# Performance work log

Hardware: AMD Instinct MI355X
Metric: run time of the kernel (lower is better)

Reference implementation:

```python
import jax, jax.numpy as jnp
import numpy as np

NEG_SLOPE = 0.2


def gat_layer(x, src, dst, W, a_src, a_dst, b, n_nodes):
    # x: [N, F_in]; W: [F_in, H*C]; a_src/a_dst: [H, C]; b: [H*C]
    H, C = a_src.shape
    h = (x @ W).reshape(n_nodes, H, C)                    # [N, H, C]
    al_s = jnp.sum(h * a_src, axis=-1)                    # [N, H]
    al_d = jnp.sum(h * a_dst, axis=-1)                    # [N, H]
    e = jax.nn.leaky_relu(al_s[src] + al_d[dst], NEG_SLOPE)  # [E, H]
    # segment softmax over incoming edges of each dst node
    m = jax.ops.segment_max(e, dst, num_segments=n_nodes)   # [N, H]
    e = jnp.exp(e - m[dst])
    s = jax.ops.segment_sum(e, dst, num_segments=n_nodes)   # [N, H]
    alpha = e / (s[dst] + 1e-16)                             # [E, H]
    msg = h[src] * alpha[:, :, None]                         # [E, H, C]
    out = jax.ops.segment_sum(msg, dst, num_segments=n_nodes)
    return out.reshape(n_nodes, H * C) + b


def setup_inputs() -> dict:
    key = jax.random.key(0)
    ks = jax.random.split(key, 16)
    N, E = 50000, 800000
    F_in, Hd, heads, n_cls = 256, 256, 8, 64
    C = Hd // heads
    x = jax.random.normal(ks[0], (N, F_in), dtype=jnp.float32)
    edge_index = jax.random.randint(ks[1], (2, E), 0, N, dtype=jnp.int64)

    def lin(k, fin, fout):
        return jax.random.normal(k, (fin, fout), dtype=jnp.float32) / np.sqrt(fin).astype(np.float32)

    inp = {"x": x, "edge_index": edge_index}
    # layer 1: 256 -> 8 heads x 32
    inp["W1"] = lin(ks[2], F_in, Hd)
    inp["as1"] = jax.random.normal(ks[3], (heads, C), dtype=jnp.float32) * 0.1
    inp["ad1"] = jax.random.normal(ks[4], (heads, C), dtype=jnp.float32) * 0.1
    inp["b1"] = jnp.zeros((Hd,), dtype=jnp.float32)
    # layer 2: 256 -> 8 heads x 32
    inp["W2"] = lin(ks[5], Hd, Hd)
    inp["as2"] = jax.random.normal(ks[6], (heads, C), dtype=jnp.float32) * 0.1
    inp["ad2"] = jax.random.normal(ks[7], (heads, C), dtype=jnp.float32) * 0.1
    inp["b2"] = jnp.zeros((Hd,), dtype=jnp.float32)
    # layer 3: 256 -> 1 head x 64 (num_classes)
    inp["W3"] = lin(ks[8], Hd, n_cls)
    inp["as3"] = jax.random.normal(ks[9], (1, n_cls), dtype=jnp.float32) * 0.1
    inp["ad3"] = jax.random.normal(ks[10], (1, n_cls), dtype=jnp.float32) * 0.1
    inp["b3"] = jnp.zeros((n_cls,), dtype=jnp.float32)
    return inp


def reference(x, edge_index, W1, as1, ad1, b1, W2, as2, ad2, b2, W3, as3, ad3, b3):
    N = x.shape[0]
    # PyG GATConv default add_self_loops=True
    loop = jnp.arange(N, dtype=edge_index.dtype)
    src = jnp.concatenate([edge_index[0], loop])
    dst = jnp.concatenate([edge_index[1], loop])
    h = gat_layer(x, src, dst, W1, as1, ad1, b1, N)
    h = jax.nn.relu(h)  # dropout is identity at inference
    h = gat_layer(h, src, dst, W2, as2, ad2, b2, N)
    h = jax.nn.relu(h)
    out = gat_layer(h, src, dst, W3, as3, ad3, b3, N)
    return out
```

## Files before the change

kernel.cpp:

```cpp
#include <hip/hip_runtime.h>
#include <math.h>

#define NSLOPE 0.2f

typedef __attribute__((ext_vector_type(8))) short bf16x8;
typedef __attribute__((ext_vector_type(8))) unsigned short ushort8;
typedef __attribute__((ext_vector_type(4))) float f32x4;

static __device__ __forceinline__ float leaky(float e) {
    return e > 0.f ? e : NSLOPE * e;
}

static __device__ __forceinline__ float bfu(unsigned short u) {
    return __uint_as_float(((unsigned)u) << 16);
}

static __device__ __forceinline__ unsigned short f2bf_rne(float f) {
    unsigned b = __float_as_uint(f);
    unsigned r = b + 0x7fffu + ((b >> 16) & 1u);
    return (unsigned short)(r >> 16);
}

static __device__ __forceinline__ void split1(float f, unsigned short& hi,
                                              unsigned short& lo) {
    unsigned b = __float_as_uint(f);
    unsigned hb = b & 0xffff0000u;
    hi = (unsigned short)(hb >> 16);
    lo = (unsigned short)(__float_as_uint(f - __uint_as_float(hb)) >> 16);
}


__global__ void k_scan_local(const int* __restrict__ cnt, int* __restrict__ ptr,
                             int* __restrict__ bsum, int N) {
    __shared__ int sd[256];
    int t = threadIdx.x;
    int i0 = blockIdx.x * 1024 + t * 4;
    int v0 = (i0 + 0 < N) ? cnt[i0 + 0] + 1 : 0;
    int v1 = (i0 + 1 < N) ? cnt[i0 + 1] + 1 : 0;
    int v2 = (i0 + 2 < N) ? cnt[i0 + 2] + 1 : 0;
    int v3 = (i0 + 3 < N) ? cnt[i0 + 3] + 1 : 0;
    int ts = v0 + v1 + v2 + v3;
    sd[t] = ts;
    __syncthreads();
    for (int o = 1; o < 256; o <<= 1) {
        int add = (t >= o) ? sd[t - o] : 0;
        __syncthreads();
        sd[t] += add;
        __syncthreads();
    }
    int run = sd[t] - ts;
    if (i0 + 0 < N) ptr[i0 + 0] = run; run += v0;
    if (i0 + 1 < N) ptr[i0 + 1] = run; run += v1;
    if (i0 + 2 < N) ptr[i0 + 2] = run; run += v2;
    if (i0 + 3 < N) ptr[i0 + 3] = run;
    if (t == 255) bsum[blockIdx.x] = sd[255];
}

__global__ void k_scan_add2(int* __restrict__ ptr, int* __restrict__ fptr,
                            const int* __restrict__ bsum, int N, int Et) {
    __shared__ int base;
    const int chunk = blockIdx.x >> 2;
    if (threadIdx.x == 0) {
        int s = 0;
        for (int b = 0; b < chunk; ++b) s += bsum[b];
        base = s;
    }
    __syncthreads();
    int i = blockIdx.x * 256 + threadIdx.x;
    if (i < N) {
        int v = ptr[i] + base;
        ptr[i] = v;
        fptr[i] = v;
    } else if (i == N) {
        ptr[N] = Et;
    }
}

__global__ void k_fillcsr(const int* __restrict__ ei, int* __restrict__ fptr,
                          int* __restrict__ srcs, int E, int Et) {
    int i = blockIdx.x * blockDim.x + threadIdx.x;
    if (i >= Et) return;
    int s, d;
    if (i < E) { s = ei[i]; d = ei[E + i]; }
    else       { s = d = i - E; }
    int pos = atomicAdd(&fptr[d], 1);
    srcs[pos] = s;
}

__global__ __launch_bounds__(256) void k_prep(
    const int* __restrict__ ei_dst, int* __restrict__ cnt, int E, int N,
    const float* __restrict__ x, unsigned short* __restrict__ xhi,
    unsigned short* __restrict__ xlo, int n8,
    const float* __restrict__ W1, unsigned short* __restrict__ w1h, unsigned short* __restrict__ w1l,
    const float* __restrict__ W2, unsigned short* __restrict__ w2h, unsigned short* __restrict__ w2l,
    const float* __restrict__ W3, unsigned short* __restrict__ w3h, unsigned short* __restrict__ w3l,
    int ncnt, int nsplit) {
    __shared__ float tile[32][33];
    const int b = blockIdx.x;
    const int tid = threadIdx.x;
    if (b < ncnt) {
        int i = b * 256 + tid;
        if (i < E) atomicAdd(&cnt[ei_dst[i]], 1);
    } else if (b < ncnt + nsplit) {
        int i = (b - ncnt) * 256 + tid;
        if (i < n8) {
            const float4 v0 = *reinterpret_cast<const float4*>(&x[(size_t)i * 8]);
            const float4 v1 = *reinterpret_cast<const float4*>(&x[(size_t)i * 8 + 4]);
            const float f[8] = {v0.x, v0.y, v0.z, v0.w, v1.x, v1.y, v1.z, v1.w};
            ushort8 h, l;
#pragma unroll
            for (int j = 0; j < 8; ++j) {
                unsigned short hj, lj;
                split1(f[j], hj, lj);
                h[j] = hj; l[j] = lj;
            }
            *reinterpret_cast<ushort8*>(&xhi[(size_t)i * 8]) = h;
            *reinterpret_cast<ushort8*>(&xlo[(size_t)i * 8]) = l;
        }
    } else {
        int tb = b - ncnt - nsplit;
        const float* B; unsigned short *H, *L;
        int M, bx, by;
        if (tb < 64)       { B = W1; H = w1h; L = w1l; M = 256; bx = (tb & 7) * 32; by = (tb >> 3) * 32; }
        else if (tb < 128) { tb -= 64;  B = W2; H = w2h; L = w2l; M = 256; bx = (tb & 7) * 32; by = (tb >> 3) * 32; }
        else               { tb -= 128; B = W3; H = w3h; L = w3l; M = 64;  bx = (tb & 1) * 32; by = (tb >> 1) * 32; }
        constexpr int K = 256;
        const int tx = tid & 31, ty = tid >> 5;
        for (int r = ty; r < 32; r += 8) tile[r][tx] = B[(size_t)(by + r) * M + bx + tx];
        __syncthreads();
        for (int r = ty; r < 32; r += 8) {
            unsigned short h, l;
            split1(tile[tx][r], h, l);
            H[(size_t)(bx + r) * K + by + tx] = h;
            L[(size_t)(bx + r) * K + by + tx] = l;
        }
    }
}

__global__ __launch_bounds__(256) void k_gemm2(const unsigned short* __restrict__ Ahi,
                                               const unsigned short* __restrict__ Alo,
                                               const unsigned short* __restrict__ Whi,
                                               const unsigned short* __restrict__ Wlo,
                                               const float* __restrict__ asrc,
                                               const float* __restrict__ adst,
                                               unsigned short* __restrict__ hb,
                                               float* __restrict__ als,
                                               float* __restrict__ ald,
                                               int N) {
    constexpr int K = 256;
    constexpr int M = 256;
    __shared__ unsigned short Ah[64][36], Al[64][36];
    __shared__ unsigned short Bh[256][36], Bl[256][36];
    const int tid = threadIdx.x;
    const int lane = tid & 63;
    const int wid = tid >> 6;
    const int row0 = blockIdx.x * 64;

    const int sr = tid >> 2;
    const int sk = (tid & 3) << 3;
    const int ga = row0 + sr;
    const size_t gaK = (size_t)ga * K;

    const int wc0 = wid * 64;
    const int fr = lane & 15;
    const int ko = (lane >> 4) * 8;

    f32x4 acc[4][4];
#pragma unroll
    for (int i = 0; i < 4; ++i)
#pragma unroll
        for (int j = 0; j < 4; ++j) acc[i][j] = (f32x4){0.f, 0.f, 0.f, 0.f};

    for (int k0 = 0; k0 < K; k0 += 32) {
        ushort8 ah = {0,0,0,0,0,0,0,0}, al = {0,0,0,0,0,0,0,0};
        if (ga < N) {
            ah = *reinterpret_cast<const ushort8*>(&Ahi[gaK + k0 + sk]);
            al = *reinterpret_cast<const ushort8*>(&Alo[gaK + k0 + sk]);
        }
        *reinterpret_cast<ushort8*>(&Ah[sr][sk]) = ah;
        *reinterpret_cast<ushort8*>(&Al[sr][sk]) = al;
#pragma unroll
        for (int p = 0; p < 4; ++p) {
            const int m = sr + 64 * p;
            const size_t gm = (size_t)m * K + k0 + sk;
            *reinterpret_cast<ushort8*>(&Bh[m][sk]) =
                *reinterpret_cast<const ushort8*>(&Whi[gm]);
            *reinterpret_cast<ushort8*>(&Bl[m][sk]) =
                *reinterpret_cast<const ushort8*>(&Wlo[gm]);
        }
        __syncthreads();

        bf16x8 ahi[4], alo4[4];
#pragma unroll
        for (int i = 0; i < 4; ++i) {
            ahi[i]  = *reinterpret_cast<const bf16x8*>(&Ah[i * 16 + fr][ko]);
            alo4[i] = *reinterpret_cast<const bf16x8*>(&Al[i * 16 + fr][ko]);
        }
#pragma unroll
        for (int j = 0; j < 4; ++j) {
            const bf16x8 bh = *reinterpret_cast<const bf16x8*>(&Bh[wc0 + j * 16 + fr][ko]);
            const bf16x8 bl = *reinterpret_cast<const bf16x8*>(&Bl[wc0 + j * 16 + fr][ko]);
#pragma unroll
            for (int i = 0; i < 4; ++i) {
                acc[i][j] = __builtin_amdgcn_mfma_f32_16x16x32_bf16(ahi[i], bh, acc[i][j], 0, 0, 0);
                acc[i][j] = __builtin_amdgcn_mfma_f32_16x16x32_bf16(ahi[i], bl, acc[i][j], 0, 0, 0);
                acc[i][j] = __builtin_amdgcn_mfma_f32_16x16x32_bf16(alo4[i], bh, acc[i][j], 0, 0, 0);
            }
        }
        __syncthreads();
    }

    const int orow = (lane >> 4) * 4;
    const int ocol = lane & 15;

#pragma unroll
    for (int i = 0; i < 4; ++i) {
#pragma unroll
        for (int r = 0; r < 4; ++r) {
            const int row = row0 + i * 16 + orow + r;
            if (row < N) {
#pragma unroll
                for (int j = 0; j < 4; ++j) {
                    const int col = wc0 + j * 16 + ocol;
                    hb[(size_t)row * M + col] = f2bf_rne(acc[i][j][r]);
                }
            }
        }
    }

    const float as0 = asrc[wc0 + ocol],      as1 = asrc[wc0 + 16 + ocol];
    const float as2 = asrc[wc0 + 32 + ocol], as3 = asrc[wc0 + 48 + ocol];
    const float ad0 = adst[wc0 + ocol],      ad1 = adst[wc0 + 16 + ocol];
    const float ad2 = adst[wc0 + 32 + ocol], ad3 = adst[wc0 + 48 + ocol];
    const int headA = wc0 >> 5, headB = headA + 1;

#pragma unroll
    for (int i = 0; i < 4; ++i) {
#pragma unroll
        for (int r = 0; r < 4; ++r) {
            float psA = acc[i][0][r] * as0 + acc[i][1][r] * as1;
            float pdA = acc[i][0][r] * ad0 + acc[i][1][r] * ad1;
            float psB = acc[i][2][r] * as2 + acc[i][3][r] * as3;
            float pdB = acc[i][2][r] * ad2 + acc[i][3][r] * ad3;
#pragma unroll
            for (int o = 1; o < 16; o <<= 1) {
                psA += __shfl_xor(psA, o);
                pdA += __shfl_xor(pdA, o);
                psB += __shfl_xor(psB, o);
                pdB += __shfl_xor(pdB, o);
            }
            const int row = row0 + i * 16 + orow + r;
            if (ocol == 0 && row < N) {
                als[(size_t)row * 8 + headA] = psA;
                ald[(size_t)row * 8 + headA] = pdA;
                als[(size_t)row * 8 + headB] = psB;
                ald[(size_t)row * 8 + headB] = pdB;
            }
        }
    }
}


template <int HN, int CN>
__global__ __launch_bounds__(256) void k_gemm_s(const unsigned short* __restrict__ Ahi,
                                                const unsigned short* __restrict__ Alo,
                                                const unsigned short* __restrict__ Whi,
                                                const unsigned short* __restrict__ Wlo,
                                                const float* __restrict__ asrc,
                                                const float* __restrict__ adst,
                                                unsigned short* __restrict__ hb,
                                                float* __restrict__ als,
                                                float* __restrict__ ald,
                                                int N) {
    constexpr int K = 256;
    constexpr int M = HN * CN;
    __shared__ unsigned short Ah[64][40], Al[64][40], Bh[64][40], Bl[64][40];
    const int tid = threadIdx.x;
    const int lane = tid & 63;
    const int wid = tid >> 6;
    const int row0 = blockIdx.x * 64;
    const int col0 = blockIdx.y * 64;

    const int sr = tid >> 2;
    const int sk = (tid & 3) << 3;
    const int ga = row0 + sr;
    const size_t gaK = (size_t)ga * K;
    const size_t gcK = (size_t)(col0 + sr) * K;

    const int wr = (wid >> 1) * 32;
    const int wc = (wid & 1) * 32;
    const int fr = lane & 15;
    const int ko = (lane >> 4) * 8;

    f32x4 acc[2][2];
#pragma unroll
    for (int i = 0; i < 2; ++i)
#pragma unroll
        for (int j = 0; j < 2; ++j) acc[i][j] = (f32x4){0.f, 0.f, 0.f, 0.f};

    for (int k0 = 0; k0 < K; k0 += 32) {
        ushort8 ah = {0,0,0,0,0,0,0,0}, al = {0,0,0,0,0,0,0,0};
        if (ga < N) {
            ah = *reinterpret_cast<const ushort8*>(&Ahi[gaK + k0 + sk]);
            al = *reinterpret_cast<const ushort8*>(&Alo[gaK + k0 + sk]);
        }
        const ushort8 bh = *reinterpret_cast<const ushort8*>(&Whi[gcK + k0 + sk]);
        const ushort8 bl = *reinterpret_cast<const ushort8*>(&Wlo[gcK + k0 + sk]);
        *reinterpret_cast<ushort8*>(&Ah[sr][sk]) = ah;
        *reinterpret_cast<ushort8*>(&Al[sr][sk]) = al;
        *reinterpret_cast<ushort8*>(&Bh[sr][sk]) = bh;
        *reinterpret_cast<ushort8*>(&Bl[sr][sk]) = bl;
        __syncthreads();

        bf16x8 ahi[2], alo[2], bhi[2], blo[2];
#pragma unroll
        for (int i = 0; i < 2; ++i) {
            ahi[i] = *reinterpret_cast<const bf16x8*>(&Ah[wr + i * 16 + fr][ko]);
            alo[i] = *reinterpret_cast<const bf16x8*>(&Al[wr + i * 16 + fr][ko]);
        }
#pragma unroll
        for (int j = 0; j < 2; ++j) {
            bhi[j] = *reinterpret_cast<const bf16x8*>(&Bh[wc + j * 16 + fr][ko]);
            blo[j] = *reinterpret_cast<const bf16x8*>(&Bl[wc + j * 16 + fr][ko]);
        }
#pragma unroll
        for (int i = 0; i < 2; ++i)
#pragma unroll
            for (int j = 0; j < 2; ++j) {
                acc[i][j] = __builtin_amdgcn_mfma_f32_16x16x32_bf16(ahi[i], bhi[j], acc[i][j], 0, 0, 0);
                acc[i][j] = __builtin_amdgcn_mfma_f32_16x16x32_bf16(ahi[i], blo[j], acc[i][j], 0, 0, 0);
                acc[i][j] = __builtin_amdgcn_mfma_f32_16x16x32_bf16(alo[i], bhi[j], acc[i][j], 0, 0, 0);
            }
        __syncthreads();
    }

    const int orow = (lane >> 4) * 4;
    const int ocol = lane & 15;

#pragma unroll
    for (int i = 0; i < 2; ++i) {
#pragma unroll
        for (int r = 0; r < 4; ++r) {
            const int row = row0 + wr + i * 16 + orow + r;
            if (row < N) {
#pragma unroll
                for (int j = 0; j < 2; ++j) {
                    const int col = col0 + wc + j * 16 + ocol;
                    hb[(size_t)row * M + col] = f2bf_rne(acc[i][j][r]);
                }
            }
        }
    }

    const int c0 = col0 + wc;
    const float as0 = asrc[c0 + ocol],      as1 = asrc[c0 + 16 + ocol];
    const float ad0 = adst[c0 + ocol],      ad1 = adst[c0 + 16 + ocol];

    {
        __shared__ float part[2][64][2];
#pragma unroll
        for (int i = 0; i < 2; ++i) {
#pragma unroll
            for (int r = 0; r < 4; ++r) {
                float ps = acc[i][0][r] * as0 + acc[i][1][r] * as1;
                float pd = acc[i][0][r] * ad0 + acc[i][1][r] * ad1;
#pragma unroll
                for (int o = 1; o < 16; o <<= 1) {
                    ps += __shfl_xor(ps, o);
                    pd += __shfl_xor(pd, o);
                }
                if (ocol == 0) {
                    const int lr = wr + i * 16 + orow + r;
                    part[wc >> 5][lr][0] = ps;
                    part[wc >> 5][lr][1] = pd;
                }
            }
        }
        __syncthreads();
        if (tid < 64) {
            const int row = row0 + tid;
            if (row < N) {
                als[row] = part[0][tid][0] + part[1][tid][0];
                ald[row] = part[0][tid][1] + part[1][tid][1];
            }
        }
    }
}

template <int HN, int CN, int VEC, int P, bool OSPLIT>
__global__ __launch_bounds__(256) void k_agg6(const unsigned short* __restrict__ hb,
                                              const float* __restrict__ als,
                                              const float* __restrict__ ald,
                                              const int* __restrict__ ptr,
                                              const int* __restrict__ srcs,
                                              const float* __restrict__ bias,
                                              unsigned short* __restrict__ ohi,
                                              unsigned short* __restrict__ olo,
                                              float* __restrict__ out,
                                              int N, int relu) {
    constexpr int HC = HN * CN;
    constexpr int SUBS = 64 / HN;
    constexpr int GB = (SUBS < 16) ? SUBS : 16;
    const int l = threadIdx.x & 63;
    const int n = blockIdx.x * 4 + (threadIdx.x >> 6);
    if (n >= N) return;
    const int beg = ptr[n], end = ptr[n + 1];
    const int hd_e = l % HN;
    const int sub = l / HN;
    const float aldv = ald[(unsigned)n * HN + hd_e];

    float p[P];
    int   sr[P];
    float ssum = 0.f;
#pragma unroll
    for (int b = 0; b < P; ++b) {
        const int j = beg + b * SUBS + sub;
        float pv = 0.f; int s = 0;
        if (j < end) {
            s = srcs[j];
            pv = __expf(leaky(als[(unsigned)s * HN + hd_e] + aldv));
        }
        sr[b] = s; p[b] = pv; ssum += pv;
    }
    for (int j = beg + P * SUBS + sub; j < end; j += SUBS) {
        ssum += __expf(leaky(als[(unsigned)srcs[j] * HN + hd_e] + aldv));
    }
#pragma unroll
    for (int o = HN; o < 64; o <<= 1) ssum += __shfl_xor(ssum, o);
    const float inv = 1.f / (ssum + 1e-16f);

    const int ch = l * VEC;
    const int hl = ch / CN;
    float acc[VEC];
#pragma unroll
    for (int v = 0; v < VEC; ++v) acc[v] = 0.f;

#pragma unroll
    for (int b = 0; b < P; ++b) {
        const int j0 = beg + b * SUBS;
        if (j0 >= end) break;
        const float am = p[b] * inv;
#pragma unroll
        for (int cb = 0; cb < SUBS / GB; ++cb) {
            if (j0 + cb * GB >= end) break;
            float av[GB];
            if constexpr (VEC == 4) {
                ushort4 hv[GB];
#pragma unroll
                for (int c = 0; c < GB; ++c) {
                    const int ce = cb * GB + c;
                    const int s = __shfl(sr[b], ce * HN);
                    av[c] = __shfl(am, ce * HN + hl);
                    hv[c] = *reinterpret_cast<const ushort4*>(&hb[(unsigned)s * HC + ch]);
                }
#pragma unroll
                for (int c = 0; c < GB; ++c) {
                    acc[0] += av[c] * bfu(hv[c].x);
                    acc[1] += av[c] * bfu(hv[c].y);
                    acc[2] += av[c] * bfu(hv[c].z);
                    acc[3] += av[c] * bfu(hv[c].w);
                }
            } else {
                unsigned short hv[GB];
#pragma unroll
                for (int c = 0; c < GB; ++c) {
                    const int ce = cb * GB + c;
                    const int s = __shfl(sr[b], ce * HN);
                    av[c] = __shfl(am, ce * HN + hl);
                    hv[c] = hb[(unsigned)s * HC + ch];
                }
#pragma unroll
                for (int c = 0; c < GB; ++c) acc[0] += av[c] * bfu(hv[c]);
            }
        }
    }
    for (int j0 = beg + P * SUBS; j0 < end; j0 += SUBS) {
        const int j = j0 + sub;
        int sm = 0; float am = 0.f;
        if (j < end) {
            sm = srcs[j];
            am = __expf(leaky(als[(unsigned)sm * HN + hd_e] + aldv)) * inv;
        }
#pragma unroll
        for (int cb = 0; cb < SUBS / GB; ++cb) {
            if (j0 + cb * GB >= end) break;
            float av[GB];
            if constexpr (VEC == 4) {
                ushort4 hv[GB];
#pragma unroll
                for (int c = 0; c < GB; ++c) {
                    const int ce = cb * GB + c;
                    const int s = __shfl(sm, ce * HN);
                    av[c] = __shfl(am, ce * HN + hl);
                    hv[c] = *reinterpret_cast<const ushort4*>(&hb[(unsigned)s * HC + ch]);
                }
#pragma unroll
                for (int c = 0; c < GB; ++c) {
                    acc[0] += av[c] * bfu(hv[c].x);
                    acc[1] += av[c] * bfu(hv[c].y);
                    acc[2] += av[c] * bfu(hv[c].z);
                    acc[3] += av[c] * bfu(hv[c].w);
                }
            } else {
                unsigned short hv[GB];
#pragma unroll
                for (int c = 0; c < GB; ++c) {
                    const int ce = cb * GB + c;
                    const int s = __shfl(sm, ce * HN);
                    av[c] = __shfl(am, ce * HN + hl);
                    hv[c] = hb[(unsigned)s * HC + ch];
                }
#pragma unroll
                for (int c = 0; c < GB; ++c) acc[0] += av[c] * bfu(hv[c]);
            }
        }
    }

#pragma unroll
    for (int v = 0; v < VEC; ++v) {
        float o = acc[v] + bias[ch + v];
        if (relu) o = fmaxf(o, 0.f);
        acc[v] = o;
    }
    if constexpr (OSPLIT) {
        ushort4 ho, lo4;
        unsigned short h0, l0;
        split1(acc[0], h0, l0); ho.x = h0; lo4.x = l0;
        split1(acc[1], h0, l0); ho.y = h0; lo4.y = l0;
        split1(acc[2], h0, l0); ho.z = h0; lo4.z = l0;
        split1(acc[3], h0, l0); ho.w = h0; lo4.w = l0;
        *reinterpret_cast<ushort4*>(&ohi[(unsigned)n * HC + ch]) = ho;
        *reinterpret_cast<ushort4*>(&olo[(unsigned)n * HC + ch]) = lo4;
    } else if constexpr (VEC == 4) {
        float4 vout;
        vout.x = acc[0]; vout.y = acc[1]; vout.z = acc[2]; vout.w = acc[3];
        *reinterpret_cast<float4*>(&out[(unsigned)n * HC + ch]) = vout;
    } else {
        out[(unsigned)n * HC + ch] = acc[0];
    }
}

template <int P>
__global__ __launch_bounds__(256) void k_agg7(const unsigned short* __restrict__ hb,
                                              const float* __restrict__ als,
                                              const float* __restrict__ ald,
                                              const int* __restrict__ ptr,
                                              const int* __restrict__ srcs,
                                              const float* __restrict__ bias,
                                              float* __restrict__ out,
                                              int N) {
    constexpr int HC = 64;
    const int l = threadIdx.x & 63;
    const int n = blockIdx.x * 4 + (threadIdx.x >> 6);
    if (n >= N) return;
    const int beg = ptr[n], end = ptr[n + 1];
    const float aldv = ald[n];

    float p[P];
    int   sr[P];
    float ssum = 0.f;
#pragma unroll
    for (int b = 0; b < P; ++b) {
        const int j = beg + b * 64 + l;
        float pv = 0.f; int s = 0;
        if (j < end) { s = srcs[j]; pv = __expf(leaky(als[s] + aldv)); }
        sr[b] = s; p[b] = pv; ssum += pv;
    }
    for (int j = beg + P * 64 + l; j < end; j += 64)
        ssum += __expf(leaky(als[srcs[j]] + aldv));
#pragma unroll
    for (int o = 1; o < 64; o <<= 1) ssum += __shfl_xor(ssum, o);
    const float inv = 1.f / (ssum + 1e-16f);

    const int grp = l >> 4;
    const int lch = (l & 15) * 4;
    float acc[4] = {0.f, 0.f, 0.f, 0.f};

#pragma unroll
    for (int b = 0; b < P; ++b) {
        const int j0 = beg + b * 64;
        if (j0 >= end) break;
        const float am = p[b] * inv;
        const int ned = min(64, end - j0);
        const int nblk = (ned + 15) >> 4;
        for (int cb = 0; cb < nblk; ++cb) {
            const int e0 = cb * 16 + grp;
            const float a0 = __shfl(am, e0),       a1 = __shfl(am, e0 + 4);
            const float a2 = __shfl(am, e0 + 8),   a3 = __shfl(am, e0 + 12);
            const int   s0 = __shfl(sr[b], e0),      s1 = __shfl(sr[b], e0 + 4);
            const int   s2 = __shfl(sr[b], e0 + 8),  s3 = __shfl(sr[b], e0 + 12);
            const ushort4 h0 = *reinterpret_cast<const ushort4*>(&hb[(unsigned)s0 * HC + lch]);
            const ushort4 h1 = *reinterpret_cast<const ushort4*>(&hb[(unsigned)s1 * HC + lch]);
            const ushort4 h2 = *reinterpret_cast<const ushort4*>(&hb[(unsigned)s2 * HC + lch]);
            const ushort4 h3 = *reinterpret_cast<const ushort4*>(&hb[(unsigned)s3 * HC + lch]);
            acc[0] += a0 * bfu(h0.x) + a1 * bfu(h1.x) + a2 * bfu(h2.x) + a3 * bfu(h3.x);
            acc[1] += a0 * bfu(h0.y) + a1 * bfu(h1.y) + a2 * bfu(h2.y) + a3 * bfu(h3.y);
            acc[2] += a0 * bfu(h0.z) + a1 * bfu(h1.z) + a2 * bfu(h2.z) + a3 * bfu(h3.z);
            acc[3] += a0 * bfu(h0.w) + a1 * bfu(h1.w) + a2 * bfu(h2.w) + a3 * bfu(h3.w);
        }
    }
    for (int j0 = beg + P * 64; j0 < end; j0 += 64) {
        const int j = j0 + l;
        int sm = 0; float am = 0.f;
        if (j < end) { sm = srcs[j]; am = __expf(leaky(als[sm] + aldv)) * inv; }
        const int ned = min(64, end - j0);
        const int nblk = (ned + 15) >> 4;
        for (int cb = 0; cb < nblk; ++cb) {
            const int e0 = cb * 16 + grp;
            const float a0 = __shfl(am, e0),       a1 = __shfl(am, e0 + 4);
            const float a2 = __shfl(am, e0 + 8),   a3 = __shfl(am, e0 + 12);
            const int   s0 = __shfl(sm, e0),       s1 = __shfl(sm, e0 + 4);
            const int   s2 = __shfl(sm, e0 + 8),   s3 = __shfl(sm, e0 + 12);
            const ushort4 h0 = *reinterpret_cast<const ushort4*>(&hb[(unsigned)s0 * HC + lch]);
            const ushort4 h1 = *reinterpret_cast<const ushort4*>(&hb[(unsigned)s1 * HC + lch]);
            const ushort4 h2 = *reinterpret_cast<const ushort4*>(&hb[(unsigned)s2 * HC + lch]);
            const ushort4 h3 = *reinterpret_cast<const ushort4*>(&hb[(unsigned)s3 * HC + lch]);
            acc[0] += a0 * bfu(h0.x) + a1 * bfu(h1.x) + a2 * bfu(h2.x) + a3 * bfu(h3.x);
            acc[1] += a0 * bfu(h0.y) + a1 * bfu(h1.y) + a2 * bfu(h2.y) + a3 * bfu(h3.y);
            acc[2] += a0 * bfu(h0.z) + a1 * bfu(h1.z) + a2 * bfu(h2.z) + a3 * bfu(h3.z);
            acc[3] += a0 * bfu(h0.w) + a1 * bfu(h1.w) + a2 * bfu(h2.w) + a3 * bfu(h3.w);
        }
    }

#pragma unroll
    for (int o = 16; o < 64; o <<= 1) {
#pragma unroll
        for (int v = 0; v < 4; ++v) acc[v] += __shfl_xor(acc[v], o);
    }

    if (l < 16) {
        float4 vout;
        vout.x = acc[0] + bias[lch + 0];
        vout.y = acc[1] + bias[lch + 1];
        vout.z = acc[2] + bias[lch + 2];
        vout.w = acc[3] + bias[lch + 3];
        *reinterpret_cast<float4*>(&out[(size_t)n * HC + lch]) = vout;
    }
}


extern "C" void kernel_launch(void* const* d_in, const int* in_sizes, int n_in,
                              void* d_out, int out_size, void* d_ws, size_t ws_size,
                              hipStream_t stream) {
    const float* x   = (const float*)d_in[0];
    const int*   ei  = (const int*)d_in[1];
    const float* W1  = (const float*)d_in[2];
    const float* as1 = (const float*)d_in[3];
    const float* ad1 = (const float*)d_in[4];
    const float* b1  = (const float*)d_in[5];
    const float* W2  = (const float*)d_in[6];
    const float* as2 = (const float*)d_in[7];
    const float* ad2 = (const float*)d_in[8];
    const float* b2  = (const float*)d_in[9];
    const float* W3  = (const float*)d_in[10];
    const float* as3 = (const float*)d_in[11];
    const float* ad3 = (const float*)d_in[12];
    const float* b3  = (const float*)d_in[13];

    const int F  = 256;
    const int N  = in_sizes[0] / F;
    const int E  = in_sizes[1] / 2;
    const int Et = E + N;

    char* w = (char*)d_ws;
    auto alloc = [&](size_t bytes) {
        char* p = w;
        w += (bytes + 255) & ~(size_t)255;
        return p;
    };
    unsigned short* S0hi = (unsigned short*)alloc((size_t)N * F * 2);
    unsigned short* S0lo = (unsigned short*)alloc((size_t)N * F * 2);
    unsigned short* S1hi = (unsigned short*)alloc((size_t)N * F * 2);
    unsigned short* S1lo = (unsigned short*)alloc((size_t)N * F * 2);
    unsigned short* hB   = (unsigned short*)alloc((size_t)N * F * 2);
    unsigned short* Wt1hi = (unsigned short*)alloc((size_t)256 * 256 * 2);
    unsigned short* Wt1lo = (unsigned short*)alloc((size_t)256 * 256 * 2);
    unsigned short* Wt2hi = (unsigned short*)alloc((size_t)256 * 256 * 2);
    unsigned short* Wt2lo = (unsigned short*)alloc((size_t)256 * 256 * 2);
    unsigned short* Wt3hi = (unsigned short*)alloc((size_t)64 * 256 * 2);
    unsigned short* Wt3lo = (unsigned short*)alloc((size_t)64 * 256 * 2);
    float* als  = (float*)alloc((size_t)N * 8 * 4);
    float* ald  = (float*)alloc((size_t)N * 8 * 4);
    int*   cnt  = (int*)alloc((size_t)N * 4);
    int*   ptr  = (int*)alloc((size_t)(N + 1) * 4);
    int*   fptr = (int*)alloc((size_t)(N + 1) * 4);
    int*   srcs = (int*)alloc((size_t)Et * 4);
    int*   bsum = (int*)alloc(4096);

    const int n8 = N * F / 8;
    const int ncnt = (E + 255) / 256;
    const int nsplit = (n8 + 255) / 256;
    const int nprep = ncnt + nsplit + 64 + 64 + 16;

    hipMemsetAsync(cnt, 0, (size_t)N * 4, stream);
    hipLaunchKernelGGL(k_prep, dim3(nprep), dim3(256), 0, stream,
                       ei + E, cnt, E, N, x, S0hi, S0lo, n8,
                       W1, Wt1hi, Wt1lo, W2, Wt2hi, Wt2lo, W3, Wt3hi, Wt3lo,
                       ncnt, nsplit);

    const int nb = (N + 1023) / 1024;
    hipLaunchKernelGGL(k_scan_local,dim3(nb),               dim3(256), 0, stream, cnt, ptr, bsum, N);
    hipLaunchKernelGGL(k_scan_add2, dim3((N + 256) / 256),  dim3(256), 0, stream, ptr, fptr, bsum, N, Et);
    hipLaunchKernelGGL(k_fillcsr,   dim3((Et + 255) / 256), dim3(256), 0, stream, ei, fptr, srcs, E, Et);

    const dim3 gN4((N + 3) / 4);
    const int gx = (N + 63) / 64;

    hipLaunchKernelGGL(k_gemm2, dim3(gx), dim3(256), 0, stream,
                       S0hi, S0lo, Wt1hi, Wt1lo, as1, ad1, hB, als, ald, N);
    hipLaunchKernelGGL((k_agg6<8, 32, 4, 8, true>), gN4, dim3(256), 0, stream,
                       hB, als, ald, ptr, srcs, b1, S1hi, S1lo, nullptr, N, 1);
    hipLaunchKernelGGL(k_gemm2, dim3(gx), dim3(256), 0, stream,
                       S1hi, S1lo, Wt2hi, Wt2lo, as2, ad2, hB, als, ald, N);
    hipLaunchKernelGGL((k_agg6<8, 32, 4, 8, true>), gN4, dim3(256), 0, stream,
                       hB, als, ald, ptr, srcs, b2, S0hi, S0lo, nullptr, N, 1);
    hipLaunchKernelGGL((k_gemm_s<1, 64>), dim3(gx, 1), dim3(256), 0, stream,
                       S0hi, S0lo, Wt3hi, Wt3lo, as3, ad3, hB, als, ald, N);
    hipLaunchKernelGGL((k_agg7<2>), gN4, dim3(256), 0, stream,
                       hB, als, ald, ptr, srcs, b3, (float*)d_out, N);
}
```

Baseline: 385.4 us.

## Store activations as single bf16 instead of hi/lo split pairs

Activations (the input x and the intermediate layer outputs) are now rounded to a single bf16 instead of split into hi+lo bf16 pairs. This halves activation write and read traffic and removes one of the three MFMAs per tile in both GEMMs. Weights keep their hi/lo split. The edge counting moves out of k_prep into its own kernel launch, and the templates are simplified. The risk is lower accuracy, since activations lose about 8 mantissa bits, which could affect tolerance.

```diff
diff --git a/kernel.cpp b/kernel.cpp
--- a/kernel.cpp
+++ b/kernel.cpp
@@ -29,6 +29,11 @@
     lo = (unsigned short)(__float_as_uint(f - __uint_as_float(hb)) >> 16);
 }
 
+
+__global__ void k_count(const int* __restrict__ dst, int* __restrict__ cnt, int E) {
+    int i = blockIdx.x * blockDim.x + threadIdx.x;
+    if (i < E) atomicAdd(&cnt[dst[i]], 1);
+}
 
 __global__ void k_scan_local(const int* __restrict__ cnt, int* __restrict__ ptr,
                              int* __restrict__ bsum, int N) {
@@ -88,37 +93,27 @@
 }
 
 __global__ __launch_bounds__(256) void k_prep(
-    const int* __restrict__ ei_dst, int* __restrict__ cnt, int E, int N,
-    const float* __restrict__ x, unsigned short* __restrict__ xhi,
-    unsigned short* __restrict__ xlo, int n8,
+    const float* __restrict__ x, unsigned short* __restrict__ xb, int n8,
     const float* __restrict__ W1, unsigned short* __restrict__ w1h, unsigned short* __restrict__ w1l,
     const float* __restrict__ W2, unsigned short* __restrict__ w2h, unsigned short* __restrict__ w2l,
     const float* __restrict__ W3, unsigned short* __restrict__ w3h, unsigned short* __restrict__ w3l,
-    int ncnt, int nsplit) {
+    int nsplit) {
     __shared__ float tile[32][33];
     const int b = blockIdx.x;
     const int tid = threadIdx.x;
-    if (b < ncnt) {
+    if (b < nsplit) {
         int i = b * 256 + tid;
-        if (i < E) atomicAdd(&cnt[ei_dst[i]], 1);
-    } else if (b < ncnt + nsplit) {
-        int i = (b - ncnt) * 256 + tid;
         if (i < n8) {
             const float4 v0 = *reinterpret_cast<const float4*>(&x[(size_t)i * 8]);
             const float4 v1 = *reinterpret_cast<const float4*>(&x[(size_t)i * 8 + 4]);
             const float f[8] = {v0.x, v0.y, v0.z, v0.w, v1.x, v1.y, v1.z, v1.w};
-            ushort8 h, l;
-#pragma unroll
-            for (int j = 0; j < 8; ++j) {
-                unsigned short hj, lj;
-                split1(f[j], hj, lj);
-                h[j] = hj; l[j] = lj;
-            }
-            *reinterpret_cast<ushort8*>(&xhi[(size_t)i * 8]) = h;
-            *reinterpret_cast<ushort8*>(&xlo[(size_t)i * 8]) = l;
+            ushort8 h;
+#pragma unroll
+            for (int j = 0; j < 8; ++j) h[j] = f2bf_rne(f[j]);
+            *reinterpret_cast<ushort8*>(&xb[(size_t)i * 8]) = h;
         }
     } else {
-        int tb = b - ncnt - nsplit;
+        int tb = b - nsplit;
         const float* B; unsigned short *H, *L;
         int M, bx, by;
         if (tb < 64)       { B = W1; H = w1h; L = w1l; M = 256; bx = (tb & 7) * 32; by = (tb >> 3) * 32; }
@@ -137,8 +132,7 @@
     }
 }
 
-__global__ __launch_bounds__(256) void k_gemm2(const unsigned short* __restrict__ Ahi,
-                                               const unsigned short* __restrict__ Alo,
+__global__ __launch_bounds__(256) void k_gemm2(const unsigned short* __restrict__ Ab,
                                                const unsigned short* __restrict__ Whi,
                                                const unsigned short* __restrict__ Wlo,
                                                const float* __restrict__ asrc,
@@ -149,7 +143,7 @@
                                                int N) {
     constexpr int K = 256;
     constexpr int M = 256;
-    __shared__ unsigned short Ah[64][36], Al[64][36];
+    __shared__ unsigned short Ah[64][36];
     __shared__ unsigned short Bh[256][36], Bl[256][36];
     const int tid = threadIdx.x;
     const int lane = tid & 63;
@@ -172,13 +166,9 @@
         for (int j = 0; j < 4; ++j) acc[i][j] = (f32x4){0.f, 0.f, 0.f, 0.f};
 
     for (int k0 = 0; k0 < K; k0 += 32) {
-        ushort8 ah = {0,0,0,0,0,0,0,0}, al = {0,0,0,0,0,0,0,0};
-        if (ga < N) {
-            ah = *reinterpret_cast<const ushort8*>(&Ahi[gaK + k0 + sk]);
-            al = *reinterpret_cast<const ushort8*>(&Alo[gaK + k0 + sk]);
-        }
+        ushort8 ah = {0,0,0,0,0,0,0,0};
+        if (ga < N) ah = *reinterpret_cast<const ushort8*>(&Ab[gaK + k0 + sk]);
         *reinterpret_cast<ushort8*>(&Ah[sr][sk]) = ah;
-        *reinterpret_cast<ushort8*>(&Al[sr][sk]) = al;
 #pragma unroll
         for (int p = 0; p < 4; ++p) {
             const int m = sr + 64 * p;
@@ -190,21 +180,18 @@
         }
         __syncthreads();
 
-        bf16x8 ahi[4], alo4[4];
-#pragma unroll
-        for (int i = 0; i < 4; ++i) {
-            ahi[i]  = *reinterpret_cast<const bf16x8*>(&Ah[i * 16 + fr][ko]);
-            alo4[i] = *reinterpret_cast<const bf16x8*>(&Al[i * 16 + fr][ko]);
-        }
+        bf16x8 av[4];
+#pragma unroll
+        for (int i = 0; i < 4; ++i)
+            av[i] = *reinterpret_cast<const bf16x8*>(&Ah[i * 16 + fr][ko]);
 #pragma unroll
         for (int j = 0; j < 4; ++j) {
             const bf16x8 bh = *reinterpret_cast<const bf16x8*>(&Bh[wc0 + j * 16 + fr][ko]);
             const bf16x8 bl = *reinterpret_cast<const bf16x8*>(&Bl[wc0 + j * 16 + fr][ko]);
 #pragma unroll
             for (int i = 0; i < 4; ++i) {
-                acc[i][j] = __builtin_amdgcn_mfma_f32_16x16x32_bf16(ahi[i], bh, acc[i][j], 0, 0, 0);
-                acc[i][j] = __builtin_amdgcn_mfma_f32_16x16x32_bf16(ahi[i], bl, acc[i][j], 0, 0, 0);
-                acc[i][j] = __builtin_amdgcn_mfma_f32_16x16x32_bf16(alo4[i], bh, acc[i][j], 0, 0, 0);
+                acc[i][j] = __builtin_amdgcn_mfma_f32_16x16x32_bf16(av[i], bh, acc[i][j], 0, 0, 0);
+                acc[i][j] = __builtin_amdgcn_mfma_f32_16x16x32_bf16(av[i], bl, acc[i][j], 0, 0, 0);
             }
         }
         __syncthreads();
@@ -261,9 +248,7 @@
 }
 
 
-template <int HN, int CN>
-__global__ __launch_bounds__(256) void k_gemm_s(const unsigned short* __restrict__ Ahi,
-                                                const unsigned short* __restrict__ Alo,
+__global__ __launch_bounds__(256) void k_gemm_s(const unsigned short* __restrict__ Ab,
                                                 const unsigned short* __restrict__ Whi,
                                                 const unsigned short* __restrict__ Wlo,
                                                 const float* __restrict__ asrc,
@@ -273,19 +258,18 @@
                                                 float* __restrict__ ald,
                                                 int N) {
     constexpr int K = 256;
-    constexpr int M = HN * CN;
-    __shared__ unsigned short Ah[64][40], Al[64][40], Bh[64][40], Bl[64][40];
+    constexpr int M = 64;
+    __shared__ unsigned short Ah[64][40], Bh[64][40], Bl[64][40];
     const int tid = threadIdx.x;
     const int lane = tid & 63;
     const int wid = tid >> 6;
     const int row0 = blockIdx.x * 64;
-    const int col0 = blockIdx.y * 64;
 
     const int sr = tid >> 2;
     const int sk = (tid & 3) << 3;
     const int ga = row0 + sr;
     const size_t gaK = (size_t)ga * K;
-    const size_t gcK = (size_t)(col0 + sr) * K;
+    const size_t gcK = (size_t)sr * K;
 
     const int wr = (wid >> 1) * 32;
     const int wc = (wid & 1) * 32;
@@ -299,37 +283,30 @@
         for (int j = 0; j < 2; ++j) acc[i][j] = (f32x4){0.f, 0.f, 0.f, 0.f};
 
     for (int k0 = 0; k0 < K; k0 += 32) {
-        ushort8 ah = {0,0,0,0,0,0,0,0}, al = {0,0,0,0,0,0,0,0};
-        if (ga < N) {
-            ah = *reinterpret_cast<const ushort8*>(&Ahi[gaK + k0 + sk]);
-            al = *reinterpret_cast<const ushort8*>(&Alo[gaK + k0 + sk]);
-        }
+        ushort8 ah = {0,0,0,0,0,0,0,0};
+        if (ga < N) ah = *reinterpret_cast<const ushort8*>(&Ab[gaK + k0 + sk]);
         const ushort8 bh = *reinterpret_cast<const ushort8*>(&Whi[gcK + k0 + sk]);
         const ushort8 bl = *reinterpret_cast<const ushort8*>(&Wlo[gcK + k0 + sk]);
         *reinterpret_cast<ushort8*>(&Ah[sr][sk]) = ah;
-        *reinterpret_cast<ushort8*>(&Al[sr][sk]) = al;
         *reinterpret_cast<ushort8*>(&Bh[sr][sk]) = bh;
         *reinterpret_cast<ushort8*>(&Bl[sr][sk]) = bl;
         __syncthreads();
 
-        bf16x8 ahi[2], alo[2], bhi[2], blo[2];
-#pragma unroll
-        for (int i = 0; i < 2; ++i) {
-            ahi[i] = *reinterpret_cast<const bf16x8*>(&Ah[wr + i * 16 + fr][ko]);
-            alo[i] = *reinterpret_cast<const bf16x8*>(&Al[wr + i * 16 + fr][ko]);
-        }
+        bf16x8 av[2], bhv[2], blv[2];
+#pragma unroll
+        for (int i = 0; i < 2; ++i)
+            av[i] = *reinterpret_cast<const bf16x8*>(&Ah[wr + i * 16 + fr][ko]);
 #pragma unroll
         for (int j = 0; j < 2; ++j) {
-            bhi[j] = *reinterpret_cast<const bf16x8*>(&Bh[wc + j * 16 + fr][ko]);
-            blo[j] = *reinterpret_cast<const bf16x8*>(&Bl[wc + j * 16 + fr][ko]);
+            bhv[j] = *reinterpret_cast<const bf16x8*>(&Bh[wc + j * 16 + fr][ko]);
+            blv[j] = *reinterpret_cast<const bf16x8*>(&Bl[wc + j * 16 + fr][ko]);
         }
 #pragma unroll
         for (int i = 0; i < 2; ++i)
 #pragma unroll
             for (int j = 0; j < 2; ++j) {
-                acc[i][j] = __builtin_amdgcn_mfma_f32_16x16x32_bf16(ahi[i], bhi[j], acc[i][j], 0, 0, 0);
-                acc[i][j] = __builtin_amdgcn_mfma_f32_16x16x32_bf16(ahi[i], blo[j], acc[i][j], 0, 0, 0);
-                acc[i][j] = __builtin_amdgcn_mfma_f32_16x16x32_bf16(alo[i], bhi[j], acc[i][j], 0, 0, 0);
+                acc[i][j] = __builtin_amdgcn_mfma_f32_16x16x32_bf16(av[i], bhv[j], acc[i][j], 0, 0, 0);
+                acc[i][j] = __builtin_amdgcn_mfma_f32_16x16x32_bf16(av[i], blv[j], acc[i][j], 0, 0, 0);
             }
         __syncthreads();
     }
@@ -345,16 +322,15 @@
             if (row < N) {
 #pragma unroll
                 for (int j = 0; j < 2; ++j) {
-                    const int col = col0 + wc + j * 16 + ocol;
+                    const int col = wc + j * 16 + ocol;
                     hb[(size_t)row * M + col] = f2bf_rne(acc[i][j][r]);
                 }
             }
         }
     }
 
-    const int c0 = col0 + wc;
-    const float as0 = asrc[c0 + ocol],      as1 = asrc[c0 + 16 + ocol];
-    const float ad0 = adst[c0 + ocol],      ad1 = adst[c0 + 16 + ocol];
+    const float as0 = asrc[wc + ocol],      as1 = asrc[wc + 16 + ocol];
+    const float ad0 = adst[wc + ocol],      ad1 = adst[wc + 16 + ocol];
 
     {
         __shared__ float part[2][64][2];
@@ -387,15 +363,14 @@
     }
 }
 
-template <int HN, int CN, int VEC, int P, bool OSPLIT>
+template <int HN, int CN, int VEC, int P, bool OBF>
 __global__ __launch_bounds__(256) void k_agg6(const unsigned short* __restrict__ hb,
                                               const float* __restrict__ als,
                                               const float* __restrict__ ald,
                                               const int* __restrict__ ptr,
                                               const int* __restrict__ srcs,
                                               const float* __restrict__ bias,
-                                              unsigned short* __restrict__ ohi,
-                                              unsigned short* __restrict__ olo,
+                                              unsigned short* __restrict__ obf,
                                               float* __restrict__ out,
                                               int N, int relu) {
     constexpr int HC = HN * CN;
@@ -444,33 +419,20 @@
         for (int cb = 0; cb < SUBS / GB; ++cb) {
             if (j0 + cb * GB >= end) break;
             float av[GB];
-            if constexpr (VEC == 4) {
-                ushort4 hv[GB];
-#pragma unroll
-                for (int c = 0; c < GB; ++c) {
-                    const int ce = cb * GB + c;
-                    const int s = __shfl(sr[b], ce * HN);
-                    av[c] = __shfl(am, ce * HN + hl);
-                    hv[c] = *reinterpret_cast<const ushort4*>(&hb[(unsigned)s * HC + ch]);
-                }
-#pragma unroll
-                for (int c = 0; c < GB; ++c) {
-                    acc[0] += av[c] * bfu(hv[c].x);
-                    acc[1] += av[c] * bfu(hv[c].y);
-                    acc[2] += av[c] * bfu(hv[c].z);
-                    acc[3] += av[c] * bfu(hv[c].w);
-                }
-            } else {
-                unsigned short hv[GB];
-#pragma unroll
-                for (int c = 0; c < GB; ++c) {
-                    const int ce = cb * GB + c;
-                    const int s = __shfl(sr[b], ce * HN);
-                    av[c] = __shfl(am, ce * HN + hl);
-                    hv[c] = hb[(unsigned)s * HC + ch];
-                }
-#pragma unroll
-                for (int c = 0; c < GB; ++c) acc[0] += av[c] * bfu(hv[c]);
+            ushort4 hv[GB];
+#pragma unroll
+            for (int c = 0; c < GB; ++c) {
+                const int ce = cb * GB + c;
+                const int s = __shfl(sr[b], ce * HN);
+                av[c] = __shfl(am, ce * HN + hl);
+                hv[c] = *reinterpret_cast<const ushort4*>(&hb[(unsigned)s * HC + ch]);
+            }
+#pragma unroll
+            for (int c = 0; c < GB; ++c) {
+                acc[0] += av[c] * bfu(hv[c].x);
+                acc[1] += av[c] * bfu(hv[c].y);
+                acc[2] += av[c] * bfu(hv[c].z);
+                acc[3] += av[c] * bfu(hv[c].w);
             }
         }
     }
@@ -485,33 +447,20 @@
         for (int cb = 0; cb < SUBS / GB; ++cb) {
             if (j0 + cb * GB >= end) break;
             float av[GB];
-            if constexpr (VEC == 4) {
-                ushort4 hv[GB];
-#pragma unroll
-                for (int c = 0; c < GB; ++c) {
-                    const int ce = cb * GB + c;
-                    const int s = __shfl(sm, ce * HN);
-                    av[c] = __shfl(am, ce * HN + hl);
-                    hv[c] = *reinterpret_cast<const ushort4*>(&hb[(unsigned)s * HC + ch]);
-                }
-#pragma unroll
-                for (int c = 0; c < GB; ++c) {
-                    acc[0] += av[c] * bfu(hv[c].x);
-                    acc[1] += av[c] * bfu(hv[c].y);
-                    acc[2] += av[c] * bfu(hv[c].z);
-                    acc[3] += av[c] * bfu(hv[c].w);
-                }
-            } else {
-                unsigned short hv[GB];
-#pragma unroll
-                for (int c = 0; c < GB; ++c) {
-                    const int ce = cb * GB + c;
-                    const int s = __shfl(sm, ce * HN);
-                    av[c] = __shfl(am, ce * HN + hl);
-                    hv[c] = hb[(unsigned)s * HC + ch];
-                }
-#pragma unroll
-                for (int c = 0; c < GB; ++c) acc[0] += av[c] * bfu(hv[c]);
+            ushort4 hv[GB];
+#pragma unroll
+            for (int c = 0; c < GB; ++c) {
+                const int ce = cb * GB + c;
+                const int s = __shfl(sm, ce * HN);
+                av[c] = __shfl(am, ce * HN + hl);
+                hv[c] = *reinterpret_cast<const ushort4*>(&hb[(unsigned)s * HC + ch]);
+            }
+#pragma unroll
+            for (int c = 0; c < GB; ++c) {
+                acc[0] += av[c] * bfu(hv[c].x);
+                acc[1] += av[c] * bfu(hv[c].y);
+                acc[2] += av[c] * bfu(hv[c].z);
+                acc[3] += av[c] * bfu(hv[c].w);
             }
         }
     }
@@ -522,21 +471,17 @@
         if (relu) o = fmaxf(o, 0.f);
         acc[v] = o;
     }
-    if constexpr (OSPLIT) {
-        ushort4 ho, lo4;
-        unsigned short h0, l0;
-        split1(acc[0], h0, l0); ho.x = h0; lo4.x = l0;
-        split1(acc[1], h0, l0); ho.y = h0; lo4.y = l0;
-        split1(acc[2], h0, l0); ho.z = h0; lo4.z = l0;
-        split1(acc[3], h0, l0); ho.w = h0; lo4.w = l0;
-        *reinterpret_cast<ushort4*>(&ohi[(unsigned)n * HC + ch]) = ho;
-        *reinterpret_cast<ushort4*>(&olo[(unsigned)n * HC + ch]) = lo4;
-    } else if constexpr (VEC == 4) {
+    if constexpr (OBF) {
+        ushort4 ho;
+        ho.x = f2bf_rne(acc[0]);
+        ho.y = f2bf_rne(acc[1]);
+        ho.z = f2bf_rne(acc[2]);
+        ho.w = f2bf_rne(acc[3]);
+        *reinterpret_cast<ushort4*>(&obf[(unsigned)n * HC + ch]) = ho;
+    } else {
         float4 vout;
         vout.x = acc[0]; vout.y = acc[1]; vout.z = acc[2]; vout.w = acc[3];
         *reinterpret_cast<float4*>(&out[(unsigned)n * HC + ch]) = vout;
-    } else {
-        out[(unsigned)n * HC + ch] = acc[0];
     }
 }
 
@@ -668,10 +613,8 @@
         w += (bytes + 255) & ~(size_t)255;
         return p;
     };
-    unsigned short* S0hi = (unsigned short*)alloc((size_t)N * F * 2);
-    unsigned short* S0lo = (unsigned short*)alloc((size_t)N * F * 2);
-    unsigned short* S1hi = (unsigned short*)alloc((size_t)N * F * 2);
-    unsigned short* S1lo = (unsigned short*)alloc((size_t)N * F * 2);
+    unsigned short* xb   = (unsigned short*)alloc((size_t)N * F * 2);
+    unsigned short* act1 = (unsigned short*)alloc((size_t)N * F * 2);
     unsigned short* hB   = (unsigned short*)alloc((size_t)N * F * 2);
     unsigned short* Wt1hi = (unsigned short*)alloc((size_t)256 * 256 * 2);
     unsigned short* Wt1lo = (unsigned short*)alloc((size_t)256 * 256 * 2);
@@ -688,17 +631,17 @@
     int*   bsum = (int*)alloc(4096);
 
     const int n8 = N * F / 8;
-    const int ncnt = (E + 255) / 256;
     const int nsplit = (n8 + 255) / 256;
-    const int nprep = ncnt + nsplit + 64 + 64 + 16;
+    const int nprep = nsplit + 64 + 64 + 16;
 
     hipMemsetAsync(cnt, 0, (size_t)N * 4, stream);
     hipLaunchKernelGGL(k_prep, dim3(nprep), dim3(256), 0, stream,
-                       ei + E, cnt, E, N, x, S0hi, S0lo, n8,
+                       x, xb, n8,
                        W1, Wt1hi, Wt1lo, W2, Wt2hi, Wt2lo, W3, Wt3hi, Wt3lo,
-                       ncnt, nsplit);
+                       nsplit);
 
     const int nb = (N + 1023) / 1024;
+    hipLaunchKernelGGL(k_count,     dim3((E + 255) / 256),  dim3(256), 0, stream, ei + E, cnt, E);
     hipLaunchKernelGGL(k_scan_local,dim3(nb),               dim3(256), 0, stream, cnt, ptr, bsum, N);
     hipLaunchKernelGGL(k_scan_add2, dim3((N + 256) / 256),  dim3(256), 0, stream, ptr, fptr, bsum, N, Et);
     hipLaunchKernelGGL(k_fillcsr,   dim3((Et + 255) / 256), dim3(256), 0, stream, ei, fptr, srcs, E, Et);
@@ -707,15 +650,15 @@
     const int gx = (N + 63) / 64;
 
     hipLaunchKernelGGL(k_gemm2, dim3(gx), dim3(256), 0, stream,
-                       S0hi, S0lo, Wt1hi, Wt1lo, as1, ad1, hB, als, ald, N);
+                       xb, Wt1hi, Wt1lo, as1, ad1, hB, als, ald, N);
     hipLaunchKernelGGL((k_agg6<8, 32, 4, 8, true>), gN4, dim3(256), 0, stream,
-                       hB, als, ald, ptr, srcs, b1, S1hi, S1lo, nullptr, N, 1);
+                       hB, als, ald, ptr, srcs, b1, act1, nullptr, N, 1);
     hipLaunchKernelGGL(k_gemm2, dim3(gx), dim3(256), 0, stream,
-                       S1hi, S1lo, Wt2hi, Wt2lo, as2, ad2, hB, als, ald, N);
+                       act1, Wt2hi, Wt2lo, as2, ad2, hB, als, ald, N);
     hipLaunchKernelGGL((k_agg6<8, 32, 4, 8, true>), gN4, dim3(256), 0, stream,
-                       hB, als, ald, ptr, srcs, b2, S0hi, S0lo, nullptr, N, 1);
-    hipLaunchKernelGGL((k_gemm_s<1, 64>), dim3(gx, 1), dim3(256), 0, stream,
-                       S0hi, S0lo, Wt3hi, Wt3lo, as3, ad3, hB, als, ald, N);
+                       hB, als, ald, ptr, srcs, b2, xb, nullptr, N, 1);
+    hipLaunchKernelGGL(k_gemm_s, dim3(gx), dim3(256), 0, stream,
+                       xb, Wt3hi, Wt3lo, as3, ad3, hB, als, ald, N);
     hipLaunchKernelGGL((k_agg7<2>), gN4, dim3(256), 0, stream,
                        hB, als, ald, ptr, srcs, b3, (float*)d_out, N);
 }
```

Result: faster. 367.6 us (-4.6%).
